# Kernel tuning notes

Measured on AMD Instinct MI355X. Metric: run time of the kernel, lower is better.

Reference implementation:

```python
import jax, jax.numpy as jnp
import numpy as np
from jax import lax

NUM_NEURONS = 144
NUM_E = 115  # int(144 * 0.8)
NEURONS_PER_CELL = 16
TAU = 2.0
V_TH = 1.0

# action -> (dx, dy) -> grid cell -> neuron slice; precomputed 5x144 current table
_ACTION_TO_POS = {0: (1, 0), 1: (0, -1), 2: (-1, 0), 3: (0, 1), 4: (0, 0)}

def _build_action_table():
    tab = np.zeros((5, NUM_NEURONS), dtype=np.float32)
    for a, (dx, dy) in _ACTION_TO_POS.items():
        x, y = 1 + dx, 1 + dy
        if 0 <= x < 3 and 0 <= y < 3:
            cell = y * 3 + x
            tab[a, cell * NEURONS_PER_CELL:(cell + 1) * NEURONS_PER_CELL] = 5.0
    return jnp.asarray(tab)

_EI_MASK = jnp.concatenate([jnp.ones(NUM_E, jnp.float32), -jnp.ones(NUM_NEURONS - NUM_E, jnp.float32)])


def setup_inputs() -> dict:
    key = jax.random.key(0)
    k1, k2, k3, k4 = jax.random.split(key, 4)
    B, NB = 16384, 8
    actions = jax.random.randint(k1, (B,), 0, 5)
    neighbor_E_spikes = (jax.random.uniform(k2, (B, NB, NUM_E)) < 0.2).astype(jnp.float32)
    W_rec = jax.random.normal(k3, (NUM_NEURONS, NUM_NEURONS), jnp.float32) * 0.01
    mask = jax.random.uniform(jax.random.fold_in(k3, 1), (NUM_NEURONS, NUM_NEURONS)) >= 0.9
    W_rec = W_rec * mask.astype(jnp.float32)
    W_inh = jax.random.normal(k4, (NUM_NEURONS, NUM_E), jnp.float32) * 0.1
    return {"actions": actions, "neighbor_E_spikes": neighbor_E_spikes,
            "W_rec": W_rec, "W_inh": W_inh, "num_ticks": 30}


def reference(actions, neighbor_E_spikes, W_rec, W_inh, num_ticks):
    B = actions.shape[0]
    input_current = _build_action_table()[actions]  # [B, 144]
    # neighbor loop == sum over neighbors, constant across ticks
    inhibition = jnp.einsum('bne,oe->bo', neighbor_E_spikes, W_inh)  # [B, 144]
    const_drive = 0.5 * input_current - 0.5 * inhibition

    def step(carry, _):
        v, acc = carry
        rec = (acc @ W_rec.T) * _EI_MASK          # recurrent input with Dale mask
        x = const_drive + 0.3 * rec
        v = v + (x - v) / TAU                      # LIF charge (decay_input=True, v_reset=0)
        s = (v >= V_TH).astype(v.dtype)            # spike
        v = v * (1.0 - s)                          # hard reset to 0
        return (v, acc + s), None

    init = (jnp.zeros((B, NUM_NEURONS), jnp.float32), jnp.zeros((B, NUM_NEURONS), jnp.float32))
    (_, acc), _ = lax.scan(step, init, None, length=num_ticks)
    return acc[:, :NUM_E]
```

## Files before the change

### kernel.cpp

```cpp
#include <hip/hip_runtime.h>
#include <string.h>


#define NN 144
#define NE 115
#define NB 32
#define THREADS 512
#define SLOTS 9

#define STREAM_BASE 4096
#define META_STRIDE 32

__device__ __forceinline__ float u2f(unsigned u) {
    float f; memcpy(&f, &u, 4); return f;
}

__global__ void prep_kernel(const float* __restrict__ W_rec,
                            int* __restrict__ meta, char* __restrict__ wsB) {
    __shared__ int cnt[NN], sorted[NN];
    __shared__ int pkp[72], pOff[72];
    __shared__ int wBase[8];
    const int t = threadIdx.x;

    for (int i = t; i < 28672 / 4; i += 256) ((int*)(wsB + STREAM_BASE))[i] = 0;

    if (t < NN) {
        int c = 0;
        for (int j = 0; j < NN; ++j) c += (W_rec[t * NN + j] != 0.0f);
        cnt[t] = c;
    }
    __syncthreads();
    if (t < NN) {
        int ct = cnt[t], r = 0;
        for (int j = 0; j < NN; ++j) {
            int cj = cnt[j];
            r += (cj > ct) || (cj == ct && j < t);
        }
        sorted[r] = t;
    }
    __syncthreads();
    if (t == 0) {
        int wsum[8][SLOTS];
        for (int i = 0; i < 72; ++i) {
            int c0 = cnt[sorted[2 * i]], c1 = cnt[sorted[2 * i + 1]];
            int mx = c0 > c1 ? c0 : c1; if (mx < 1) mx = 1;
            pkp[i] = (mx + 3) & ~3;
            int r = i / 8, pos = i % 8;
            int w = (r & 1) ? (7 - pos) : pos;
            wsum[w][r] = i;
        }
        int off = 0;
        for (int w = 0; w < 8; ++w) {
            wBase[w] = off;
            for (int r = 0; r < SLOTS; ++r) {
                int p = wsum[w][r];
                pOff[p] = off;
                off += pkp[p] * 16;
            }
            for (int r = 0; r < SLOTS; ++r) {
                int p = wsum[w][r];
                meta[w * META_STRIDE + 1 + r * 3]     = pkp[p];
                meta[w * META_STRIDE + 1 + r * 3 + 1] = sorted[2 * p];
                meta[w * META_STRIDE + 1 + r * 3 + 2] = sorted[2 * p + 1];
            }
            meta[w * META_STRIDE] = wBase[w];
        }
    }
    __syncthreads();
    if (t < 144) {
        int i = t >> 1, h = t & 1;
        int row = sorted[2 * i + h];
        char* base = wsB + STREAM_BASE + pOff[i] + h * 32;
        int k = 0;
        for (int j = 0; j < NN; ++j) {
            float w = W_rec[row * NN + j];
            if (w != 0.0f) {
                int c = k >> 2, pos = k & 3;
                char* a = base + c * 64 + (pos >= 2 ? 16 : 0) + (pos & 1) * 8;
                *(unsigned*)a     = (unsigned)j * 128u;
                *(float*)(a + 4)  = w;
                ++k;
            }
        }
    }
}

#define GF4(S0, S1)                                                     \
    {                                                                   \
        float a0 = *(const float*)(ldsB + ((S0).x + lro));              \
        float a1 = *(const float*)(ldsB + ((S0).z + lro));              \
        float a2 = *(const float*)(ldsB + ((S1).x + lro));              \
        float a3 = *(const float*)(ldsB + ((S1).z + lro));              \
        rec += (double)u2f((S0).y) * (double)a0;                        \
        rec += (double)u2f((S0).w) * (double)a1;                        \
        rec += (double)u2f((S1).y) * (double)a2;                        \
        rec += (double)u2f((S1).w) * (double)a3;                        \
    }

__global__ __launch_bounds__(THREADS) void snn_kernel(
        const int*   __restrict__ actions,
        const float* __restrict__ spk,
        const float* __restrict__ W_inh,
        const int*   __restrict__ meta,
        const char*  __restrict__ wsB,
        const int*   __restrict__ nt_ptr,
        float*       __restrict__ out,
        int B) {
    __shared__ float accF[2][NN * NB];
    __shared__ int   metaL[8 * META_STRIDE];

    const char* ldsB = (const char*)&accF[0][0];
    float*      nbF  = &accF[1][0];

    const int t    = threadIdx.x;
    const int lane = t & 63;
    const int wid  = t >> 6;
    const int h    = lane >> 5;
    const int bb   = lane & 31;
    const int b0   = blockIdx.x * NB;
    const int b    = b0 + bb;
    const int ticks = *nt_ptr;

    int vz;
    asm volatile("v_mov_b32 %0, 0" : "=v"(vz));

    if (t < 8 * META_STRIDE) metaL[t] = meta[t];

    for (int p = t; p < NB * NE; p += THREADS) {
        int bb2 = p / NE;
        int e   = p - bb2 * NE;
        float s = 0.0f;
        if (b0 + bb2 < B) {
            const float* sp = spk + ((size_t)(b0 + bb2) * 8) * NE + e;
            #pragma unroll
            for (int n = 0; n < 8; ++n) s += sp[n * NE];
        }
        nbF[e * NB + bb2] = s;
    }
    for (int i = t; i < NN * NB; i += THREADS) accF[0][i] = 0.0f;
    __syncthreads();

    const int mBase = wid * META_STRIDE;
    const int sbase = __builtin_amdgcn_readfirstlane(metaL[mBase]);
    int skp[SLOTS], rows[SLOTS];
    #pragma unroll
    for (int r = 0; r < SLOTS; ++r) {
        skp[r]  = __builtin_amdgcn_readfirstlane(metaL[mBase + 1 + r * 3]);
        rows[r] = metaL[mBase + 1 + r * 3 + 1 + h];
    }

    double drv[SLOTS];
    {
        int a = (b < B) ? actions[b] : 4;
        int cs = ((a == 0) ? 5 : (a == 1) ? 1 : (a == 2) ? 3 : (a == 3) ? 7 : 4) * 16;
        #pragma unroll
        for (int r = 0; r < SLOTS; ++r) {
            double inh = 0.0;
            for (int e = 0; e < NE; ++e)
                inh += (double)nbF[e * NB + bb] * (double)W_inh[rows[r] * NE + e];
            double ic = (rows[r] >= cs && rows[r] < cs + 16) ? 5.0 : 0.0;
            drv[r] = 0.5 * ic - 0.5 * inh;
        }
    }

    const uint4* pBase = (const uint4*)(wsB + STREAM_BASE + sbase) + (h << 1) + vz;

    double v[SLOTS];
    float  accv[SLOTS];
    #pragma unroll
    for (int r = 0; r < SLOTS; ++r) { v[r] = 0.0; accv[r] = 0.0f; }

    for (int tk = 0; tk < ticks; ++tk) {
        __syncthreads();
        const unsigned rbOff = (tk & 1) ? 18432u : 0u;
        const unsigned lro   = (unsigned)(bb * 4) + rbOff;
        char* WbB = (char*)ldsB + ((tk & 1) ? 0u : 18432u);

        const uint4* q = pBase;
        uint4 SA0 = q[0], SA1 = q[1];
        uint4 SB0 = q[4], SB1 = q[5];

        #pragma unroll
        for (int r = 0; r < SLOTS; ++r) {
            double rec = 0.0;
            int k = 0;
            const int kend = skp[r];
            while (k + 8 <= kend) {
                GF4(SA0, SA1);
                SA0 = q[8];  SA1 = q[9];
                GF4(SB0, SB1);
                SB0 = q[12]; SB1 = q[13];
                q += 8; k += 8;
            }
            if (k < kend) {
                GF4(SA0, SA1);
                SA0 = SB0; SA1 = SB1;
                SB0 = q[8]; SB1 = q[9];
                q += 4;
            }
            const int o = rows[r];
            double x = drv[r] + 0.3 * ((o < NE) ? rec : -rec);
            double vv = v[r];
            vv += (x - vv) * 0.5;
            double sd = (vv >= 1.0) ? 1.0 : 0.0;
            vv *= (1.0 - sd);
            v[r] = vv;
            accv[r] += (float)sd;
            *(float*)(WbB + (unsigned)o * 128u + bb * 4) = accv[r];
        }
    }

    if (b < B) {
        #pragma unroll
        for (int r = 0; r < SLOTS; ++r) {
            int o = rows[r];
            if (o < NE) out[(size_t)b * NE + o] = accv[r];
        }
    }
}

extern "C" void kernel_launch(void* const* d_in, const int* in_sizes, int n_in,
                              void* d_out, int out_size, void* d_ws, size_t ws_size,
                              hipStream_t stream) {
    const int*   actions = (const int*)  d_in[0];
    const float* spk     = (const float*)d_in[1];
    const float* W_rec   = (const float*)d_in[2];
    const float* W_inh   = (const float*)d_in[3];
    const int*   nt      = (const int*)  d_in[4];
    float* out = (float*)d_out;
    int B = in_sizes[0];

    int*  meta = (int*)d_ws;
    char* wsB  = (char*)d_ws;

    prep_kernel<<<1, 256, 0, stream>>>(W_rec, meta, wsB);
    int nblocks = (B + NB - 1) / NB;
    snn_kernel<<<nblocks, THREADS, 0, stream>>>(actions, spk, W_inh, meta, wsB,
                                                nt, out, B);
}
```

Baseline: 403.4 us.

## Give each wave whole rows over 64 batch lanes with a per-row CSR stream

Batch elements per block double from 32 to 64 and the block grows to 1024 threads in 16 waves. Each wave now owns nine full rows, with all 64 lanes working on different batch elements, instead of splitting two rows across half-waves. The sparse weight stream is rebuilt as one contiguous CSR run per row, so the index/weight loads are uniform across the wave, and rows are no longer padded to the longer of a pair. The cost is twice the LDS per block and more threads per block, which may cut register headroom and occupancy given the double-precision per-row state.

```diff
diff --git a/kernel.cpp b/kernel.cpp
--- a/kernel.cpp
+++ b/kernel.cpp
@@ -4,9 +4,9 @@
 
 #define NN 144
 #define NE 115
-#define NB 32
-#define THREADS 512
+#define NB 64
 #define SLOTS 9
+#define THREADS 1024
 
 #define STREAM_BASE 4096
 #define META_STRIDE 32
@@ -17,12 +17,10 @@
 
 __global__ void prep_kernel(const float* __restrict__ W_rec,
                             int* __restrict__ meta, char* __restrict__ wsB) {
-    __shared__ int cnt[NN], sorted[NN];
-    __shared__ int pkp[72], pOff[72];
-    __shared__ int wBase[8];
+    __shared__ int cnt[NN], sorted[NN], rowOff[NN];
     const int t = threadIdx.x;
 
-    for (int i = t; i < 28672 / 4; i += 256) ((int*)(wsB + STREAM_BASE))[i] = 0;
+    for (int i = t; i < 49152 / 4; i += 256) ((int*)(wsB + STREAM_BASE))[i] = 0;
 
     if (t < NN) {
         int c = 0;
@@ -40,52 +38,38 @@
     }
     __syncthreads();
     if (t == 0) {
-        int wsum[8][SLOTS];
-        for (int i = 0; i < 72; ++i) {
-            int c0 = cnt[sorted[2 * i]], c1 = cnt[sorted[2 * i + 1]];
-            int mx = c0 > c1 ? c0 : c1; if (mx < 1) mx = 1;
-            pkp[i] = (mx + 3) & ~3;
-            int r = i / 8, pos = i % 8;
-            int w = (r & 1) ? (7 - pos) : pos;
-            wsum[w][r] = i;
-        }
         int off = 0;
-        for (int w = 0; w < 8; ++w) {
-            wBase[w] = off;
+        for (int w = 0; w < 16; ++w) {
+            int* m = meta + w * META_STRIDE;
+            m[0] = off;
             for (int r = 0; r < SLOTS; ++r) {
-                int p = wsum[w][r];
-                pOff[p] = off;
-                off += pkp[p] * 16;
-            }
-            for (int r = 0; r < SLOTS; ++r) {
-                int p = wsum[w][r];
-                meta[w * META_STRIDE + 1 + r * 3]     = pkp[p];
-                meta[w * META_STRIDE + 1 + r * 3 + 1] = sorted[2 * p];
-                meta[w * META_STRIDE + 1 + r * 3 + 2] = sorted[2 * p + 1];
-            }
-            meta[w * META_STRIDE] = wBase[w];
-        }
-    }
-    __syncthreads();
-    if (t < 144) {
-        int i = t >> 1, h = t & 1;
-        int row = sorted[2 * i + h];
-        char* base = wsB + STREAM_BASE + pOff[i] + h * 32;
+                int pos = (r & 1) ? (15 - w) : w;
+                int row = sorted[r * 16 + pos];
+                int c = cnt[row];
+                int kp = ((c < 1 ? 1 : c) + 3) & ~3;
+                m[1 + r]  = row;
+                m[10 + r] = kp;
+                rowOff[row] = off;
+                off += kp;
+            }
+        }
+    }
+    __syncthreads();
+    if (t < NN) {
+        char* base = wsB + STREAM_BASE + (size_t)rowOff[t] * 8;
         int k = 0;
         for (int j = 0; j < NN; ++j) {
-            float w = W_rec[row * NN + j];
+            float w = W_rec[t * NN + j];
             if (w != 0.0f) {
-                int c = k >> 2, pos = k & 3;
-                char* a = base + c * 64 + (pos >= 2 ? 16 : 0) + (pos & 1) * 8;
-                *(unsigned*)a     = (unsigned)j * 128u;
-                *(float*)(a + 4)  = w;
+                *(unsigned*)(base + (size_t)k * 8)     = (unsigned)j * 256u;
+                *(float*)(base + (size_t)k * 8 + 4)    = w;
                 ++k;
             }
         }
     }
 }
 
-#define GF4(S0, S1)                                                     \
+#define GFMA4(S0, S1)                                                   \
     {                                                                   \
         float a0 = *(const float*)(ldsB + ((S0).x + lro));              \
         float a1 = *(const float*)(ldsB + ((S0).z + lro));              \
@@ -102,51 +86,49 @@
         const float* __restrict__ spk,
         const float* __restrict__ W_inh,
         const int*   __restrict__ meta,
-        const char*  __restrict__ wsB,
+        const uint4* __restrict__ csrQ,
         const int*   __restrict__ nt_ptr,
         float*       __restrict__ out,
         int B) {
     __shared__ float accF[2][NN * NB];
-    __shared__ int   metaL[8 * META_STRIDE];
+    __shared__ int   metaL[16 * META_STRIDE];
 
     const char* ldsB = (const char*)&accF[0][0];
-    float*      nbF  = &accF[1][0];
+    float* nbF = &accF[1][0];
 
     const int t    = threadIdx.x;
     const int lane = t & 63;
     const int wid  = t >> 6;
-    const int h    = lane >> 5;
-    const int bb   = lane & 31;
     const int b0   = blockIdx.x * NB;
-    const int b    = b0 + bb;
+    const int b    = b0 + lane;
     const int ticks = *nt_ptr;
 
     int vz;
     asm volatile("v_mov_b32 %0, 0" : "=v"(vz));
 
-    if (t < 8 * META_STRIDE) metaL[t] = meta[t];
+    if (t < 16 * META_STRIDE) metaL[t] = meta[t];
 
     for (int p = t; p < NB * NE; p += THREADS) {
-        int bb2 = p / NE;
-        int e   = p - bb2 * NE;
+        int bb = p / NE;
+        int e  = p - bb * NE;
         float s = 0.0f;
-        if (b0 + bb2 < B) {
-            const float* sp = spk + ((size_t)(b0 + bb2) * 8) * NE + e;
+        if (b0 + bb < B) {
+            const float* sp = spk + ((size_t)(b0 + bb) * 8) * NE + e;
             #pragma unroll
             for (int n = 0; n < 8; ++n) s += sp[n * NE];
         }
-        nbF[e * NB + bb2] = s;
+        nbF[e * (NB + 1) + bb] = s;
     }
     for (int i = t; i < NN * NB; i += THREADS) accF[0][i] = 0.0f;
     __syncthreads();
 
-    const int mBase = wid * META_STRIDE;
-    const int sbase = __builtin_amdgcn_readfirstlane(metaL[mBase]);
-    int skp[SLOTS], rows[SLOTS];
+    const int mb = wid * META_STRIDE;
+    const int sbase = __builtin_amdgcn_readfirstlane(metaL[mb]);
+    int rows[SLOTS], skp[SLOTS];
     #pragma unroll
     for (int r = 0; r < SLOTS; ++r) {
-        skp[r]  = __builtin_amdgcn_readfirstlane(metaL[mBase + 1 + r * 3]);
-        rows[r] = metaL[mBase + 1 + r * 3 + 1 + h];
+        rows[r] = __builtin_amdgcn_readfirstlane(metaL[mb + 1 + r]);
+        skp[r]  = __builtin_amdgcn_readfirstlane(metaL[mb + 10 + r]);
     }
 
     double drv[SLOTS];
@@ -157,13 +139,14 @@
         for (int r = 0; r < SLOTS; ++r) {
             double inh = 0.0;
             for (int e = 0; e < NE; ++e)
-                inh += (double)nbF[e * NB + bb] * (double)W_inh[rows[r] * NE + e];
+                inh += (double)nbF[e * (NB + 1) + lane]
+                     * (double)W_inh[rows[r] * NE + e];
             double ic = (rows[r] >= cs && rows[r] < cs + 16) ? 5.0 : 0.0;
             drv[r] = 0.5 * ic - 0.5 * inh;
         }
     }
 
-    const uint4* pBase = (const uint4*)(wsB + STREAM_BASE + sbase) + (h << 1) + vz;
+    const uint4* pBase = csrQ + (sbase >> 1) + vz;
 
     double v[SLOTS];
     float  accv[SLOTS];
@@ -172,13 +155,13 @@
 
     for (int tk = 0; tk < ticks; ++tk) {
         __syncthreads();
-        const unsigned rbOff = (tk & 1) ? 18432u : 0u;
-        const unsigned lro   = (unsigned)(bb * 4) + rbOff;
-        char* WbB = (char*)ldsB + ((tk & 1) ? 0u : 18432u);
-
-        const uint4* q = pBase;
-        uint4 SA0 = q[0], SA1 = q[1];
-        uint4 SB0 = q[4], SB1 = q[5];
+        const unsigned rbOff = (tk & 1) ? 36864u : 0u;
+        const unsigned lro   = (unsigned)(lane * 4) + rbOff;
+        char* WbB = (char*)ldsB + ((tk & 1) ? 0u : 36864u);
+
+        const uint4* p = pBase;
+        uint4 SA0 = p[0], SA1 = p[1];
+        uint4 SB0 = p[2], SB1 = p[3];
 
         #pragma unroll
         for (int r = 0; r < SLOTS; ++r) {
@@ -186,17 +169,17 @@
             int k = 0;
             const int kend = skp[r];
             while (k + 8 <= kend) {
-                GF4(SA0, SA1);
-                SA0 = q[8];  SA1 = q[9];
-                GF4(SB0, SB1);
-                SB0 = q[12]; SB1 = q[13];
-                q += 8; k += 8;
+                GFMA4(SA0, SA1);
+                SA0 = p[4]; SA1 = p[5];
+                GFMA4(SB0, SB1);
+                SB0 = p[6]; SB1 = p[7];
+                p += 4; k += 8;
             }
             if (k < kend) {
-                GF4(SA0, SA1);
+                GFMA4(SA0, SA1);
                 SA0 = SB0; SA1 = SB1;
-                SB0 = q[8]; SB1 = q[9];
-                q += 4;
+                SB0 = p[4]; SB1 = p[5];
+                p += 2;
             }
             const int o = rows[r];
             double x = drv[r] + 0.3 * ((o < NE) ? rec : -rec);
@@ -206,7 +189,7 @@
             vv *= (1.0 - sd);
             v[r] = vv;
             accv[r] += (float)sd;
-            *(float*)(WbB + (unsigned)o * 128u + bb * 4) = accv[r];
+            *(float*)(WbB + ((unsigned)o << 8) + lane * 4) = accv[r];
         }
     }
 
@@ -232,9 +215,10 @@
 
     int*  meta = (int*)d_ws;
     char* wsB  = (char*)d_ws;
+    const uint4* csrQ = (const uint4*)(wsB + STREAM_BASE);
 
     prep_kernel<<<1, 256, 0, stream>>>(W_rec, meta, wsB);
     int nblocks = (B + NB - 1) / NB;
-    snn_kernel<<<nblocks, THREADS, 0, stream>>>(actions, spk, W_inh, meta, wsB,
+    snn_kernel<<<nblocks, THREADS, 0, stream>>>(actions, spk, W_inh, meta, csrQ,
                                                 nt, out, B);
 }
```

After: 355.1 us (median of 2 runs). 1.14x faster.
